# Kernel optimization log

Measured on AMD Instinct MI355X. Metric: run time of the kernel, lower is better.

The kernel has to match this reference:

```python
import jax, jax.numpy as jnp
import numpy as np

ZERO_POINT = 128.0  # affine zero point for uint8-style storage


def setup_inputs() -> dict:
    key = jax.random.key(0)
    k1, k2, k3, k4 = jax.random.split(key, 4)
    B, S, IN, OUT = 4, 128, 4096, 11008
    inp = jax.random.normal(k1, (B, S, IN), dtype=jnp.float32)
    qweight = jax.random.randint(k2, (OUT, IN), 0, 256, dtype=jnp.int32)
    scale = jax.random.uniform(k3, (OUT, 1), dtype=jnp.float32) * 0.02 + 1e-4
    bias = jax.random.normal(k4, (OUT,), dtype=jnp.float32)
    return {"input": inp, "qweight": qweight, "scale": scale, "bias": bias}


def reference(input, qweight, scale, bias):
    # dequantize: per-out-channel affine, weight[o, i] = scale[o] * (q[o, i] - zp)
    weight = scale * (qweight.astype(jnp.float32) - ZERO_POINT)  # [OUT, IN]
    # F.linear(input, weight, bias) == input @ weight.T + bias
    return jnp.einsum("bsi,oi->bso", input, weight) + bias
```

## Files before the change

### kernel.cpp

```cpp
#include <hip/hip_runtime.h>
#include <hip/hip_bf16.h>


#define BM 64
#define BN 128
#define BK 64

typedef __attribute__((ext_vector_type(8))) short bf16x8;
typedef __attribute__((ext_vector_type(4))) float f32x4;
typedef __attribute__((ext_vector_type(4))) int   i32x4;

__device__ __forceinline__ unsigned short f2bf(float x) {
  __hip_bfloat16 h = __float2bfloat16(x);
  return *reinterpret_cast<unsigned short*>(&h);
}

__global__ __launch_bounds__(256)
void rowsum_kernel(const float* __restrict__ A, float* __restrict__ rs, int K) {
  const int row = blockIdx.x;
  const int tid = threadIdx.x;
  const float4* Ar = reinterpret_cast<const float4*>(A + (size_t)row * K);
  const int nv4 = K >> 2;
  float s = 0.f;
  for (int i = tid; i < nv4; i += 256) {
    float4 v = Ar[i];
    s += (v.x + v.y) + (v.z + v.w);
  }
#pragma unroll
  for (int off = 32; off > 0; off >>= 1) s += __shfl_down(s, off, 64);
  __shared__ float ws[4];
  if ((tid & 63) == 0) ws[tid >> 6] = s;
  __syncthreads();
  if (tid == 0) rs[row] = (ws[0] + ws[1]) + (ws[2] + ws[3]);
}

#define LOADS(s, ke) do {                                                   \
  a##s##_0 = *(const f32x4*)(Abase + (size_t)( 0) * K + (ke));              \
  a##s##_1 = *(const f32x4*)(Abase + (size_t)(16) * K + (ke));              \
  a##s##_2 = *(const f32x4*)(Abase + (size_t)(32) * K + (ke));              \
  a##s##_3 = *(const f32x4*)(Abase + (size_t)(48) * K + (ke));              \
  q##s##_0 = *(const i32x4*)(Qbase + (size_t)(  0) * K + (ke));             \
  q##s##_1 = *(const i32x4*)(Qbase + (size_t)( 16) * K + (ke));             \
  q##s##_2 = *(const i32x4*)(Qbase + (size_t)( 32) * K + (ke));             \
  q##s##_3 = *(const i32x4*)(Qbase + (size_t)( 48) * K + (ke));             \
  q##s##_4 = *(const i32x4*)(Qbase + (size_t)( 64) * K + (ke));             \
  q##s##_5 = *(const i32x4*)(Qbase + (size_t)( 80) * K + (ke));             \
  q##s##_6 = *(const i32x4*)(Qbase + (size_t)( 96) * K + (ke));             \
  q##s##_7 = *(const i32x4*)(Qbase + (size_t)(112) * K + (ke));             \
} while (0)

#define ST_A(b, it, reg) do {                                               \
  ushort4 h;                                                                \
  h.x = f2bf(reg.x); h.y = f2bf(reg.y); h.z = f2bf(reg.z); h.w = f2bf(reg.w); \
  *(ushort4*)&sA[b][(it)*16 + sr][swzc] = h;                                \
} while (0)

#define ST_Q(b, it, reg) do {                                               \
  ushort4 h;                                                                \
  h.x = f2bf((float)reg.x); h.y = f2bf((float)reg.y);                       \
  h.z = f2bf((float)reg.z); h.w = f2bf((float)reg.w);                       \
  *(ushort4*)&sB[b][(it)*16 + sr][swzc] = h;                                \
} while (0)

#define STORES(s, b) do {                                                   \
  ST_A(b, 0, a##s##_0); ST_A(b, 1, a##s##_1);                               \
  ST_A(b, 2, a##s##_2); ST_A(b, 3, a##s##_3);                               \
  ST_Q(b, 0, q##s##_0); ST_Q(b, 1, q##s##_1);                               \
  ST_Q(b, 2, q##s##_2); ST_Q(b, 3, q##s##_3);                               \
  ST_Q(b, 4, q##s##_4); ST_Q(b, 5, q##s##_5);                               \
  ST_Q(b, 6, q##s##_6); ST_Q(b, 7, q##s##_7);                               \
} while (0)

#define COMPUTE(b) do {                                                     \
  _Pragma("unroll")                                                         \
  for (int kk = 0; kk < BK; kk += 32) {                                     \
    const int kb  = (kk + ((lane >> 4) << 3)) ^ ((lane & 7) << 3);          \
    bf16x8 af0 = *(const bf16x8*)&sA[b][wr*32 +  0 + (lane & 15)][kb];      \
    bf16x8 af1 = *(const bf16x8*)&sA[b][wr*32 + 16 + (lane & 15)][kb];      \
    bf16x8 bv0 = *(const bf16x8*)&sB[b][wc*64 +  0 + (lane & 15)][kb];      \
    bf16x8 bv1 = *(const bf16x8*)&sB[b][wc*64 + 16 + (lane & 15)][kb];      \
    bf16x8 bv2 = *(const bf16x8*)&sB[b][wc*64 + 32 + (lane & 15)][kb];      \
    bf16x8 bv3 = *(const bf16x8*)&sB[b][wc*64 + 48 + (lane & 15)][kb];      \
    acc[0][0] = __builtin_amdgcn_mfma_f32_16x16x32_bf16(af0, bv0, acc[0][0], 0,0,0); \
    acc[0][1] = __builtin_amdgcn_mfma_f32_16x16x32_bf16(af0, bv1, acc[0][1], 0,0,0); \
    acc[0][2] = __builtin_amdgcn_mfma_f32_16x16x32_bf16(af0, bv2, acc[0][2], 0,0,0); \
    acc[0][3] = __builtin_amdgcn_mfma_f32_16x16x32_bf16(af0, bv3, acc[0][3], 0,0,0); \
    acc[1][0] = __builtin_amdgcn_mfma_f32_16x16x32_bf16(af1, bv0, acc[1][0], 0,0,0); \
    acc[1][1] = __builtin_amdgcn_mfma_f32_16x16x32_bf16(af1, bv1, acc[1][1], 0,0,0); \
    acc[1][2] = __builtin_amdgcn_mfma_f32_16x16x32_bf16(af1, bv2, acc[1][2], 0,0,0); \
    acc[1][3] = __builtin_amdgcn_mfma_f32_16x16x32_bf16(af1, bv3, acc[1][3], 0,0,0); \
  }                                                                         \
} while (0)

#define BAR() do {                                                          \
  asm volatile("s_waitcnt lgkmcnt(0)" ::: "memory");                        \
  __builtin_amdgcn_s_barrier();                                             \
} while (0)

__global__ __launch_bounds__(256, 2)
void qlinear_kernel(const float* __restrict__ A,
                    const int*   __restrict__ Q,
                    const float* __restrict__ scale,
                    const float* __restrict__ bias,
                    const float* __restrict__ rowsum,
                    float* __restrict__ C,
                    int M, int N, int K)
{
  __shared__ unsigned short sA[2][BM][BK];
  __shared__ unsigned short sB[2][BN][BK];

  const int tid  = threadIdx.x;
  const int lane = tid & 63;
  const int wave = tid >> 6;
  const int wr   = wave >> 1;
  const int wc   = wave & 1;

  const int nbm = M / BM;
  const int nwg = gridDim.x;
  int wgid = blockIdx.x;
  if ((nwg & 7) == 0) wgid = (wgid & 7) * (nwg >> 3) + (wgid >> 3);
  const int bm   = wgid % nbm;
  const int bn   = wgid / nbm;
  const int row0 = bm * BM;
  const int col0 = bn * BN;

  const int sr   = tid >> 4;
  const int scol = (tid & 15) << 2;
  const int swzc = scol ^ ((sr & 7) << 3);

  const float* Abase = A + (size_t)(row0 + sr) * K + scol;
  const int*   Qbase = Q + (size_t)(col0 + sr) * K + scol;

  f32x4 acc[2][4];
#pragma unroll
  for (int i = 0; i < 2; ++i)
#pragma unroll
    for (int j = 0; j < 4; ++j) acc[i][j] = (f32x4)0.0f;

  f32x4 a0_0, a0_1, a0_2, a0_3;
  f32x4 a1_0, a1_1, a1_2, a1_3;
  i32x4 q0_0, q0_1, q0_2, q0_3, q0_4, q0_5, q0_6, q0_7;
  i32x4 q1_0, q1_1, q1_2, q1_3, q1_4, q1_5, q1_6, q1_7;

  const int NT = K / BK;

  LOADS(0, 0);
  LOADS(1, BK);
  __builtin_amdgcn_sched_barrier(0);
  STORES(0, 0);
  BAR();

#pragma unroll 1
  for (int t = 0; t < NT; t += 2) {
    const int ke0 = (t + 2 < NT ? t + 2 : NT - 1) * BK;
    const int ke1 = (t + 3 < NT ? t + 3 : NT - 1) * BK;

    LOADS(0, ke0);
    __builtin_amdgcn_sched_barrier(0);
    COMPUTE(0);
    STORES(1, 1);
    BAR();

    LOADS(1, ke1);
    __builtin_amdgcn_sched_barrier(0);
    COMPUTE(1);
    STORES(0, 0);
    BAR();
  }

  const int cl = lane & 15;
  const int rb = row0 + wr * 32 + ((lane >> 4) << 2);
  float rs128[2][4];
#pragma unroll
  for (int mi = 0; mi < 2; ++mi)
#pragma unroll
    for (int r = 0; r < 4; ++r)
      rs128[mi][r] = 128.0f * rowsum[rb + mi * 16 + r];

#pragma unroll
  for (int ni = 0; ni < 4; ++ni) {
    const int n = col0 + wc * 64 + ni * 16 + cl;
    const float s = scale[n];
    const float b = bias[n];
#pragma unroll
    for (int mi = 0; mi < 2; ++mi) {
#pragma unroll
      for (int r = 0; r < 4; ++r) {
        C[(size_t)(rb + mi * 16 + r) * N + n] = (acc[mi][ni][r] - rs128[mi][r]) * s + b;
      }
    }
  }
}

extern "C" void kernel_launch(void* const* d_in, const int* in_sizes, int n_in,
                              void* d_out, int out_size, void* d_ws, size_t ws_size,
                              hipStream_t stream) {
  const float* inp   = (const float*)d_in[0];
  const int*   qw    = (const int*)d_in[1];
  const float* scale = (const float*)d_in[2];
  const float* bias  = (const float*)d_in[3];
  float*       out   = (float*)d_out;
  float*       rs    = (float*)d_ws;

  const int OUT = in_sizes[3];
  const int IN  = in_sizes[1] / OUT;
  const int M   = in_sizes[0] / IN;

  rowsum_kernel<<<M, 256, 0, stream>>>(inp, rs, IN);

  const int grid = (M / BM) * (OUT / BN);
  qlinear_kernel<<<grid, 256, 0, stream>>>(inp, qw, scale, bias, rs, out, M, OUT, IN);
}
```

Before: 351.3 us.

## Pre-convert A and Q to bf16 in workspace, GEMM via global_load_lds

Adds two conversion kernels that write bf16 copies of the activations and of the zero-point-subtracted weights into workspace. A new GEMM kernel then streams these with direct global-to-LDS loads through a single LDS buffer, with occupancy raised to 4 workgroups. This removes the in-loop float conversion and the rowsum correction. In exchange it adds an extra pass over the full int32 weight matrix (read 180MB, write 90MB) on every call, and it falls back to the old path when the workspace is too small.

```diff
diff --git a/kernel.cpp b/kernel.cpp
--- a/kernel.cpp
+++ b/kernel.cpp
@@ -13,6 +13,151 @@
 __device__ __forceinline__ unsigned short f2bf(float x) {
   __hip_bfloat16 h = __float2bfloat16(x);
   return *reinterpret_cast<unsigned short*>(&h);
+}
+
+#define GLOAD16(gptr, lptr)                                                  \
+  __builtin_amdgcn_global_load_lds(                                          \
+      (const __attribute__((address_space(1))) void*)(gptr),                 \
+      (__attribute__((address_space(3))) void*)(lptr), 16, 0, 0)
+
+__global__ __launch_bounds__(256)
+void cvtA_kernel(const float* __restrict__ A, unsigned short* __restrict__ Abf,
+                 int nquad) {
+  const int stride = gridDim.x * 256;
+  for (int i = blockIdx.x * 256 + threadIdx.x; i < nquad; i += stride) {
+    f32x4 v = *reinterpret_cast<const f32x4*>(A + (size_t)i * 4);
+    ushort4 h;
+    h.x = f2bf(v.x); h.y = f2bf(v.y); h.z = f2bf(v.z); h.w = f2bf(v.w);
+    *reinterpret_cast<ushort4*>(Abf + (size_t)i * 4) = h;
+  }
+}
+
+__global__ __launch_bounds__(256)
+void cvtQ_kernel(const int* __restrict__ Q, unsigned short* __restrict__ Qbf,
+                 int nquad) {
+  const int stride = gridDim.x * 256;
+  for (int i = blockIdx.x * 256 + threadIdx.x; i < nquad; i += stride) {
+    i32x4 v = *reinterpret_cast<const i32x4*>(Q + (size_t)i * 4);
+    ushort4 h;
+    h.x = f2bf((float)(v.x - 128));
+    h.y = f2bf((float)(v.y - 128));
+    h.z = f2bf((float)(v.z - 128));
+    h.w = f2bf((float)(v.w - 128));
+    *reinterpret_cast<ushort4*>(Qbf + (size_t)i * 4) = h;
+  }
+}
+
+__global__ __launch_bounds__(256, 4)
+void qgemm_kernel(const unsigned short* __restrict__ Abf,
+                  const unsigned short* __restrict__ Qbf,
+                  const float* __restrict__ scale,
+                  const float* __restrict__ bias,
+                  float* __restrict__ C,
+                  int M, int N, int K)
+{
+  __shared__ unsigned short sA[BM][BK];
+  __shared__ unsigned short sB[BN][BK];
+
+  const int tid  = threadIdx.x;
+  const int lane = tid & 63;
+  const int wave = tid >> 6;
+  const int wr   = wave >> 1;
+  const int wc   = wave & 1;
+
+  const int nbm = M / BM;
+  const int nwg = gridDim.x;
+  int wgid = blockIdx.x;
+  if ((nwg & 7) == 0) wgid = (wgid & 7) * (nwg >> 3) + (wgid >> 3);
+  const int bm   = wgid % nbm;
+  const int bn   = wgid / nbm;
+  const int row0 = bm * BM;
+  const int col0 = bn * BN;
+
+  const int rsub = lane >> 3;
+  const int col8 = ((lane & 7) ^ rsub) << 3;
+
+#define CHUNK_SETUP(j, gvar, lvar)                                           \
+  const unsigned short* gvar; unsigned short* lvar;                          \
+  {                                                                          \
+    const int c = wave * 6 + (j);                                            \
+    if (c < 8) {                                                             \
+      lvar = &sA[c * 8][0];                                                  \
+      gvar = Abf + (size_t)(row0 + c * 8 + rsub) * K + col8;                 \
+    } else {                                                                 \
+      lvar = &sB[(c - 8) * 8][0];                                            \
+      gvar = Qbf + (size_t)(col0 + (c - 8) * 8 + rsub) * K + col8;           \
+    }                                                                        \
+  }
+  CHUNK_SETUP(0, g0, l0)
+  CHUNK_SETUP(1, g1, l1)
+  CHUNK_SETUP(2, g2, l2)
+  CHUNK_SETUP(3, g3, l3)
+  CHUNK_SETUP(4, g4, l4)
+  CHUNK_SETUP(5, g5, l5)
+#undef CHUNK_SETUP
+
+  f32x4 acc[2][4];
+#pragma unroll
+  for (int i = 0; i < 2; ++i)
+#pragma unroll
+    for (int j = 0; j < 4; ++j) acc[i][j] = (f32x4)0.0f;
+
+  const int cl  = lane & 15;
+  const int kgr = (lane >> 4) << 3;
+
+  for (int kt = 0; kt < K; kt += BK) {
+    GLOAD16(g0 + kt, l0);
+    GLOAD16(g1 + kt, l1);
+    GLOAD16(g2 + kt, l2);
+    GLOAD16(g3 + kt, l3);
+    GLOAD16(g4 + kt, l4);
+    GLOAD16(g5 + kt, l5);
+    __syncthreads();
+
+#pragma unroll
+    for (int kk = 0; kk < BK; kk += 32) {
+      const int kb = kk + kgr;
+      bf16x8 af0, af1, bv0, bv1, bv2, bv3;
+      {
+        const int r0 = wr * 32 + 0  + cl;
+        const int r1 = wr * 32 + 16 + cl;
+        af0 = *(const bf16x8*)&sA[r0][kb ^ ((r0 & 7) << 3)];
+        af1 = *(const bf16x8*)&sA[r1][kb ^ ((r1 & 7) << 3)];
+        const int s0 = wc * 64 + 0  + cl;
+        const int s1 = wc * 64 + 16 + cl;
+        const int s2 = wc * 64 + 32 + cl;
+        const int s3 = wc * 64 + 48 + cl;
+        bv0 = *(const bf16x8*)&sB[s0][kb ^ ((s0 & 7) << 3)];
+        bv1 = *(const bf16x8*)&sB[s1][kb ^ ((s1 & 7) << 3)];
+        bv2 = *(const bf16x8*)&sB[s2][kb ^ ((s2 & 7) << 3)];
+        bv3 = *(const bf16x8*)&sB[s3][kb ^ ((s3 & 7) << 3)];
+      }
+      acc[0][0] = __builtin_amdgcn_mfma_f32_16x16x32_bf16(af0, bv0, acc[0][0], 0,0,0);
+      acc[0][1] = __builtin_amdgcn_mfma_f32_16x16x32_bf16(af0, bv1, acc[0][1], 0,0,0);
+      acc[0][2] = __builtin_amdgcn_mfma_f32_16x16x32_bf16(af0, bv2, acc[0][2], 0,0,0);
+      acc[0][3] = __builtin_amdgcn_mfma_f32_16x16x32_bf16(af0, bv3, acc[0][3], 0,0,0);
+      acc[1][0] = __builtin_amdgcn_mfma_f32_16x16x32_bf16(af1, bv0, acc[1][0], 0,0,0);
+      acc[1][1] = __builtin_amdgcn_mfma_f32_16x16x32_bf16(af1, bv1, acc[1][1], 0,0,0);
+      acc[1][2] = __builtin_amdgcn_mfma_f32_16x16x32_bf16(af1, bv2, acc[1][2], 0,0,0);
+      acc[1][3] = __builtin_amdgcn_mfma_f32_16x16x32_bf16(af1, bv3, acc[1][3], 0,0,0);
+    }
+    __syncthreads();
+  }
+
+  const int rb = row0 + wr * 32 + ((lane >> 4) << 2);
+#pragma unroll
+  for (int ni = 0; ni < 4; ++ni) {
+    const int n = col0 + wc * 64 + ni * 16 + cl;
+    const float s = scale[n];
+    const float b = bias[n];
+#pragma unroll
+    for (int mi = 0; mi < 2; ++mi) {
+#pragma unroll
+      for (int r = 0; r < 4; ++r) {
+        C[(size_t)(rb + mi * 16 + r) * N + n] = acc[mi][ni][r] * s + b;
+      }
+    }
+  }
 }
 
 __global__ __launch_bounds__(256)
@@ -92,19 +237,19 @@
   }                                                                         \
 } while (0)
 
-#define BAR() do {                                                          \
+#define BARX() do {                                                         \
   asm volatile("s_waitcnt lgkmcnt(0)" ::: "memory");                        \
   __builtin_amdgcn_s_barrier();                                             \
 } while (0)
 
 __global__ __launch_bounds__(256, 2)
-void qlinear_kernel(const float* __restrict__ A,
-                    const int*   __restrict__ Q,
-                    const float* __restrict__ scale,
-                    const float* __restrict__ bias,
-                    const float* __restrict__ rowsum,
-                    float* __restrict__ C,
-                    int M, int N, int K)
+void qlinear_fb_kernel(const float* __restrict__ A,
+                       const int*   __restrict__ Q,
+                       const float* __restrict__ scale,
+                       const float* __restrict__ bias,
+                       const float* __restrict__ rowsum,
+                       float* __restrict__ C,
+                       int M, int N, int K)
 {
   __shared__ unsigned short sA[2][BM][BK];
   __shared__ unsigned short sB[2][BN][BK];
@@ -148,7 +293,7 @@
   LOADS(1, BK);
   __builtin_amdgcn_sched_barrier(0);
   STORES(0, 0);
-  BAR();
+  BARX();
 
 #pragma unroll 1
   for (int t = 0; t < NT; t += 2) {
@@ -159,13 +304,13 @@
     __builtin_amdgcn_sched_barrier(0);
     COMPUTE(0);
     STORES(1, 1);
-    BAR();
+    BARX();
 
     LOADS(1, ke1);
     __builtin_amdgcn_sched_barrier(0);
     COMPUTE(1);
     STORES(0, 0);
-    BAR();
+    BARX();
   }
 
   const int cl = lane & 15;
@@ -200,14 +345,25 @@
   const float* scale = (const float*)d_in[2];
   const float* bias  = (const float*)d_in[3];
   float*       out   = (float*)d_out;
-  float*       rs    = (float*)d_ws;
 
   const int OUT = in_sizes[3];
   const int IN  = in_sizes[1] / OUT;
   const int M   = in_sizes[0] / IN;
 
-  rowsum_kernel<<<M, 256, 0, stream>>>(inp, rs, IN);
-
+  const size_t qbf_bytes = (size_t)OUT * IN * 2;
+  const size_t abf_bytes = (size_t)M * IN * 2;
   const int grid = (M / BM) * (OUT / BN);
-  qlinear_kernel<<<grid, 256, 0, stream>>>(inp, qw, scale, bias, rs, out, M, OUT, IN);
-}
+
+  if (ws_size >= qbf_bytes + abf_bytes) {
+    unsigned short* Qbf = (unsigned short*)d_ws;
+    unsigned short* Abf = (unsigned short*)((char*)d_ws + qbf_bytes);
+
+    cvtA_kernel<<<1024, 256, 0, stream>>>(inp, Abf, (M * IN) >> 2);
+    cvtQ_kernel<<<4096, 256, 0, stream>>>(qw, Qbf, (int)(((size_t)OUT * IN) >> 2));
+    qgemm_kernel<<<grid, 256, 0, stream>>>(Abf, Qbf, scale, bias, out, M, OUT, IN);
+  } else {
+    float* rs = (float*)d_ws;
+    rowsum_kernel<<<M, 256, 0, stream>>>(inp, rs, IN);
+    qlinear_fb_kernel<<<grid, 256, 0, stream>>>(inp, qw, scale, bias, rs, out, M, OUT, IN);
+  }
+}
```

Measured after the change: 351.5 us. Within noise of the previous version (+0.1%).
